# Optimization experiments

Hardware: AMD Instinct MI355X
Metric: run time of the kernel (lower is better)

The kernel has to match this reference:

```python
import jax, jax.numpy as jnp
import numpy as np

B, D, T, K = 32, 256, 1024, 8192


def setup_inputs() -> dict:
    key = jax.random.key(0)
    k1, k2 = jax.random.split(key)
    z_e = jax.random.normal(k1, (B, D, T), dtype=jnp.float32)
    # nn.Embedding init: uniform(-1/K, 1/K)
    emb = jax.random.uniform(k2, (K, D), dtype=jnp.float32, minval=-1.0 / K, maxval=1.0 / K)
    return {"z_e": z_e, "emb": emb}


def reference(z_e, emb):
    b, d, t = z_e.shape
    z_e_f = z_e.astype(jnp.float32)
    # [B, D, T] -> [B*T, D]
    flat = jnp.transpose(z_e_f, (0, 2, 1)).reshape(-1, d)
    # squared L2 distances to every codebook entry: [B*T, K]
    dists = (
        jnp.sum(flat * flat, axis=1, keepdims=True)
        + jnp.sum(emb * emb, axis=1)
        - 2.0 * flat @ emb.T
    )
    idx = jnp.argmin(dists, axis=1)  # [B*T]
    z_q = emb[idx].reshape(b, t, d)  # gather codebook entries
    z_q = jnp.transpose(z_q, (0, 2, 1))  # [B, D, T]
    e_loss = jnp.mean((jax.lax.stop_gradient(z_q) - z_e_f) ** 2)
    # straight-through estimator
    z_q_st = z_e + jax.lax.stop_gradient(z_q - z_e_f)
    return z_q_st, e_loss, idx.reshape(b, t)
```

## Files before the change

### kernel.cpp

```cpp
#include <hip/hip_runtime.h>
#include <stdint.h>

#define BB 32
#define DD 256
#define TT 1024
#define KK 8192

typedef __attribute__((ext_vector_type(2))) float f2;
typedef __attribute__((ext_vector_type(4))) float f4;
typedef __attribute__((ext_vector_type(8))) _Float16 hfrag;
typedef __attribute__((ext_vector_type(16))) float f16acc;

#if __has_builtin(__builtin_elementwise_fma)
#define PKFMA(a, b, c) __builtin_elementwise_fma(a, b, c)
#else
static __device__ __forceinline__ f2 pkfma_(f2 a, f2 b, f2 c) {
    f2 r; r.x = __fmaf_rn(a.x, b.x, c.x); r.y = __fmaf_rn(a.y, b.y, c.y); return r;
}
#define PKFMA(a, b, c) pkfma_(a, b, c)
#endif

#define GLD16(gp, lp)                                                          \
    __builtin_amdgcn_global_load_lds(                                          \
        (const __attribute__((address_space(1))) uint32_t*)(gp),               \
        (__attribute__((address_space(3))) uint32_t*)(lp), 16, 0, 0)

#define MU 3.0e-4f
#define BCAP 4096
#define LIST_CAP 1048576
#define INV512 0.001953125f


#define WS_LOSS   0
#define WS_CNT    8
#define WS_BCNT   16
#define WS_BF     1088
#define WS_AF     33856
#define WS_IDX    164928
#define WS_WIN    296000
#define WS_ZT     558144
#define WS_TMIN   34112576
#define WS_BKT    67667008
#define WS_LIST   71861312
#define WS_ZF     76055616
#define WS_EF     92832832
#define WS_NEED   97027136

__device__ __forceinline__ unsigned short h16(float x) {
    _Float16 t = (_Float16)x;
    return __builtin_bit_cast(unsigned short, t);
}

__device__ __forceinline__ float np_sq_sum256(const float* __restrict__ base, int stride) {
    float res[2];
    #pragma unroll
    for (int blk = 0; blk < 2; ++blk) {
        const int o = blk * 128;
        float r[8];
        #pragma unroll
        for (int j = 0; j < 8; ++j) {
            const float x = base[(o + j) * stride];
            r[j] = __fmul_rn(x, x);
        }
        for (int i = 8; i < 128; i += 8) {
            #pragma unroll
            for (int j = 0; j < 8; ++j) {
                const float x = base[(o + i + j) * stride];
                r[j] = __fadd_rn(r[j], __fmul_rn(x, x));
            }
        }
        res[blk] = __fadd_rn(__fadd_rn(__fadd_rn(r[0], r[1]), __fadd_rn(r[2], r[3])),
                             __fadd_rn(__fadd_rn(r[4], r[5]), __fadd_rn(r[6], r[7])));
    }
    return __fadd_rn(res[0], res[1]);
}

__global__ __launch_bounds__(256) void bsum_kernel(const float* __restrict__ emb,
                                                   float* __restrict__ Bf) {
    const int k = blockIdx.x * 256 + threadIdx.x;
    Bf[k] = np_sq_sum256(emb + (size_t)k * DD, 1);
}

__global__ __launch_bounds__(256) void asum_kernel(const float* __restrict__ z_e,
                                                   float* __restrict__ Af) {
    const int n = blockIdx.x * 256 + threadIdx.x;
    const int b = n >> 10, t = n & 1023;
    Af[n] = np_sq_sum256(z_e + ((size_t)b << 18) + t, TT);
}

__global__ __launch_bounds__(256) void fusedz_kernel(const float* __restrict__ z_e,
                                                     float* __restrict__ zt,
                                                     unsigned short* __restrict__ zf,
                                                     float* __restrict__ Af) {
    __shared__ float tile[64 * 261];
    const int tid = threadIdx.x, l = tid & 63, r = tid >> 6;
    const int n0 = blockIdx.x * 64;
    const int b = n0 >> 10, t0 = n0 & 1023;
    for (int d = r; d < DD; d += 4)
        tile[l * 261 + d] = z_e[(size_t)(b * DD + d) * TT + t0 + l];
    __syncthreads();
    {
        const int q = tid >> 2, c0 = (tid & 3) * 64;
        const float* src = &tile[q * 261 + c0];
        float* dzt = zt + (size_t)(n0 + q) * DD + c0;
        #pragma unroll
        for (int i = 0; i < 16; ++i) {
            f4 v;
            v.x = src[4 * i + 0]; v.y = src[4 * i + 1];
            v.z = src[4 * i + 2]; v.w = src[4 * i + 3];
            *(f4*)(dzt + 4 * i) = v;
        }
    }
    {
        const int g0 = n0 >> 5;
        #pragma unroll
        for (int i = 0; i < 8; ++i) {
            const int slot = tid + 256 * i;
            const int g  = slot >> 10;
            const int ks = (slot >> 6) & 15;
            const int ln = slot & 63;
            const int row = g * 32 + (ln & 31);
            const int col = ks * 16 + (ln >> 5) * 8;
            const float* s = &tile[row * 261 + col];
            ushort4 h0, h1;
            h0.x = h16(s[0]); h0.y = h16(s[1]); h0.z = h16(s[2]); h0.w = h16(s[3]);
            h1.x = h16(s[4]); h1.y = h16(s[5]); h1.z = h16(s[6]); h1.w = h16(s[7]);
            unsigned short* dst = zf + (((size_t)(g0 + g) * 16 + ks) * 64 + ln) * 8;
            *(ushort4*)dst       = h0;
            *(ushort4*)(dst + 4) = h1;
        }
    }
    if (tid < 64) Af[n0 + tid] = np_sq_sum256(&tile[tid * 261], 1);
}

__global__ __launch_bounds__(256) void convef_kernel(const float* __restrict__ emb,
                                                     unsigned short* __restrict__ ef) {
    const int slot = blockIdx.x * 256 + threadIdx.x;
    const int g = slot >> 10, ks = (slot >> 6) & 15, ln = slot & 63;
    const int k = g * 32 + (ln & 31);
    const int d = ks * 16 + (ln >> 5) * 8;
    const float* s = emb + (size_t)k * DD + d;
    const f4 v0 = *(const f4*)s;
    const f4 v1 = *(const f4*)(s + 4);
    ushort4 h0, h1;
    h0.x = h16(v0.x * 1024.0f); h0.y = h16(v0.y * 1024.0f);
    h0.z = h16(v0.z * 1024.0f); h0.w = h16(v0.w * 1024.0f);
    h1.x = h16(v1.x * 1024.0f); h1.y = h16(v1.y * 1024.0f);
    h1.z = h16(v1.z * 1024.0f); h1.w = h16(v1.w * 1024.0f);
    unsigned short* dst = ef + (size_t)slot * 8;
    *(ushort4*)dst       = h0;
    *(ushort4*)(dst + 4) = h1;
}

__device__ __forceinline__ void epi32(const f16acc acc, const float* BfLp,
                                      float (*minbuf)[17], int bfbase, int qrow,
                                      int col, float afv, int lane) {
    const f4 b0 = *(const f4*)&BfLp[bfbase];
    const f4 b1 = *(const f4*)&BfLp[bfbase + 8];
    const f4 b2 = *(const f4*)&BfLp[bfbase + 16];
    const f4 b3 = *(const f4*)&BfLp[bfbase + 24];
    float m =    __fmaf_rn(acc[0],  -INV512, b0.x);
    m = fminf(m, __fmaf_rn(acc[1],  -INV512, b0.y));
    m = fminf(m, __fmaf_rn(acc[2],  -INV512, b0.z));
    m = fminf(m, __fmaf_rn(acc[3],  -INV512, b0.w));
    m = fminf(m, __fmaf_rn(acc[4],  -INV512, b1.x));
    m = fminf(m, __fmaf_rn(acc[5],  -INV512, b1.y));
    m = fminf(m, __fmaf_rn(acc[6],  -INV512, b1.z));
    m = fminf(m, __fmaf_rn(acc[7],  -INV512, b1.w));
    m = fminf(m, __fmaf_rn(acc[8],  -INV512, b2.x));
    m = fminf(m, __fmaf_rn(acc[9],  -INV512, b2.y));
    m = fminf(m, __fmaf_rn(acc[10], -INV512, b2.z));
    m = fminf(m, __fmaf_rn(acc[11], -INV512, b2.w));
    m = fminf(m, __fmaf_rn(acc[12], -INV512, b3.x));
    m = fminf(m, __fmaf_rn(acc[13], -INV512, b3.y));
    m = fminf(m, __fmaf_rn(acc[14], -INV512, b3.z));
    m = fminf(m, __fmaf_rn(acc[15], -INV512, b3.w));
    m = fminf(m, __shfl_xor(m, 32));
    if (lane < 32) minbuf[qrow][col] = afv + m;
}

__global__ __launch_bounds__(256, 2) void mfma1_kernel(
    const unsigned short* __restrict__ zf, const unsigned short* __restrict__ ef,
    const float* __restrict__ Af, const float* __restrict__ Bf,
    float* __restrict__ tmp_min) {
    __shared__ unsigned short Bb[32768];
    __shared__ float minbuf[128][17];
    __shared__ float BfL[512];

    const int tid  = threadIdx.x;
    const int lane = tid & 63;
    const int w    = tid >> 6;
    const int l31  = lane & 31;
    const int hf   = lane >> 5;
    const int wq   = w & 1;
    const int wk   = w >> 1;
    const int qt   = blockIdx.x >> 4;
    const int kb   = blockIdx.x & 15;

    BfL[tid]       = Bf[kb * 512 + tid];
    BfL[tid + 256] = Bf[kb * 512 + 256 + tid];

    hfrag zr[2][16];
    #pragma unroll
    for (int cg = 0; cg < 2; ++cg) {
        const unsigned short* zb =
            zf + (((size_t)(qt * 4 + wq * 2 + cg) * 16) * 64 + lane) * 8;
        #pragma unroll
        for (int ks = 0; ks < 16; ++ks)
            zr[cg][ks] = *(const hfrag*)(zb + (size_t)ks * 512);
    }
    const float af0 = Af[qt * 128 + wq * 64 + l31];
    const float af1 = Af[qt * 128 + wq * 64 + 32 + l31];

    const unsigned short* esrc =
        ef + (((size_t)(kb * 16 + w) * 16) * 64 + lane) * 8;
    #pragma unroll
    for (int ks = 0; ks < 16; ++ks)
        GLD16(esrc + ks * 512, Bb + (w * 16 + ks) * 512);
    __syncthreads();

    for (int kt = 0; kt < 4; ++kt) {
        f16acc acc00 = {}, acc01 = {}, acc10 = {}, acc11 = {};
        #pragma unroll
        for (int ks = 0; ks < 16; ++ks) {
            const hfrag e0 = *(const hfrag*)(Bb + ((wk * 2 + 0) * 16 + ks) * 512 + lane * 8);
            const hfrag e1 = *(const hfrag*)(Bb + ((wk * 2 + 1) * 16 + ks) * 512 + lane * 8);
            acc00 = __builtin_amdgcn_mfma_f32_32x32x16_f16(e0, zr[0][ks], acc00, 0, 0, 0);
            acc01 = __builtin_amdgcn_mfma_f32_32x32x16_f16(e0, zr[1][ks], acc01, 0, 0, 0);
            acc10 = __builtin_amdgcn_mfma_f32_32x32x16_f16(e1, zr[0][ks], acc10, 0, 0, 0);
            acc11 = __builtin_amdgcn_mfma_f32_32x32x16_f16(e1, zr[1][ks], acc11, 0, 0, 0);
        }
        __syncthreads();
        if (kt < 3) {
            const unsigned short* esn = esrc + (size_t)(kt + 1) * 4 * 16 * 512;
            #pragma unroll
            for (int ks = 0; ks < 16; ++ks)
                GLD16(esn + ks * 512, Bb + (w * 16 + ks) * 512);
        }
        {
            const int bfb0 = kt * 128 + (wk * 2 + 0) * 32 + hf * 4;
            const int bfb1 = kt * 128 + (wk * 2 + 1) * 32 + hf * 4;
            const int qr0 = wq * 64 + l31, qr1 = wq * 64 + 32 + l31;
            const int c0 = kt * 4 + wk * 2, c1 = c0 + 1;
            epi32(acc00, BfL, minbuf, bfb0, qr0, c0, af0, lane);
            epi32(acc01, BfL, minbuf, bfb0, qr1, c0, af1, lane);
            epi32(acc10, BfL, minbuf, bfb1, qr0, c1, af0, lane);
            epi32(acc11, BfL, minbuf, bfb1, qr1, c1, af1, lane);
        }
        if (kt < 3) __syncthreads();
    }
    __syncthreads();
    {
        const int qloc = tid >> 1, h8 = (tid & 1) * 8;
        const float* mrow = &minbuf[qloc][h8];
        f4 v0, v1;
        v0.x = mrow[0]; v0.y = mrow[1]; v0.z = mrow[2]; v0.w = mrow[3];
        v1.x = mrow[4]; v1.y = mrow[5]; v1.z = mrow[6]; v1.w = mrow[7];
        float* dst = tmp_min + (size_t)(qt * 128 + qloc) * 256 + kb * 16 + h8;
        *(f4*)dst       = v0;
        *(f4*)(dst + 4) = v1;
    }
}

__global__ __launch_bounds__(256) void select_kernel(
    const float* __restrict__ tmp_min, int* __restrict__ bcnt,
    int* __restrict__ bucket, int* __restrict__ list, int* __restrict__ cnt,
    unsigned long long* __restrict__ winner) {
    const int tid = threadIdx.x, lane = tid & 63, w = tid >> 6;
    const int q = blockIdx.x * 4 + w;
    const f4 v = *(const f4*)(tmp_min + (size_t)q * 256 + lane * 4);
    float m = fminf(fminf(v.x, v.y), fminf(v.z, v.w));
    #pragma unroll
    for (int off = 1; off < 64; off <<= 1) m = fminf(m, __shfl_xor(m, off));
    const float thr = m + MU;
    if (lane == 0) winner[q] = ~0ULL;
    float vv[4] = {v.x, v.y, v.z, v.w};
    #pragma unroll
    for (int j = 0; j < 4; ++j) {
        if (vv[j] <= thr) {
            const int g = lane * 4 + j;
            const int pos = atomicAdd(&bcnt[g], 1);
            if (pos < BCAP) bucket[g * BCAP + pos] = q;
            else {
                const int op = atomicAdd(cnt, 1);
                if (op < LIST_CAP) list[op] = (q << 8) | g;
            }
        }
    }
}

__global__ __launch_bounds__(256) void rescan_bucket_kernel(
    const float* __restrict__ zt, const float* __restrict__ emb,
    const float* __restrict__ Af, const float* __restrict__ Bf,
    const int* __restrict__ bcnt, const int* __restrict__ bucket,
    unsigned long long* __restrict__ winner) {
    __shared__ float elds[256 * 33];
    __shared__ float zbuf[8][256];
    __shared__ float bfs[32];
    const int g     = blockIdx.x >> 3;
    const int slice = blockIdx.x & 7;
    const int tid = threadIdx.x, lane = tid & 63, w = tid >> 6;
    const int half = lane >> 5, l32 = lane & 31, slot = w * 2 + half;
    {
        const int k = tid >> 3, s0 = (tid & 7) * 32;
        const float* src = emb + (size_t)(g * 32 + k) * DD + s0;
        #pragma unroll
        for (int i = 0; i < 8; ++i) {
            const f4 v = *(const f4*)(src + i * 4);
            elds[(s0 + 4 * i + 0) * 33 + k] = v.x;
            elds[(s0 + 4 * i + 1) * 33 + k] = v.y;
            elds[(s0 + 4 * i + 2) * 33 + k] = v.z;
            elds[(s0 + 4 * i + 3) * 33 + k] = v.w;
        }
        if (tid < 32) bfs[tid] = Bf[g * 32 + tid];
    }
    __syncthreads();
    const int nit = min(bcnt[g], BCAP);
    const int kme = g * 32 + l32;
    for (int it = slice * 8 + slot; it < nit; it += 64) {
        const int q = bucket[g * BCAP + it];
        {
            f4* zb = (f4*)&zbuf[slot][0];
            const f4* zsrc = (const f4*)(zt + (size_t)q * DD);
            zb[l32]      = zsrc[l32];
            zb[l32 + 32] = zsrc[l32 + 32];
        }
        const float* zp = &zbuf[slot][0];
        float c = 0.0f;
        #pragma unroll 8
        for (int d = 0; d < DD; ++d)
            c = __fmaf_rn(zp[d], elds[d * 33 + l32], c);
        float bv = __fsub_rn(__fadd_rn(Af[q], bfs[l32]), __fadd_rn(c, c));
        int bk = kme;
        #pragma unroll
        for (int off = 1; off < 32; off <<= 1) {
            const float ob = __shfl_xor(bv, off);
            const int   ok = __shfl_xor(bk, off);
            if (ob < bv || (ob == bv && ok < bk)) { bv = ob; bk = ok; }
        }
        if (l32 == 0)
            atomicMin(winner + q,
                      (((unsigned long long)__float_as_uint(bv)) << 32) | (unsigned)bk);
    }
}

__global__ __launch_bounds__(256) void rescan2_kernel(
    const float* __restrict__ zt, const float* __restrict__ emb,
    const float* __restrict__ Af, const float* __restrict__ Bf,
    const int* __restrict__ list, const int* __restrict__ cnt,
    unsigned long long* __restrict__ winner) {
    __shared__ float zbuf[8][256];
    const int tid = threadIdx.x, lane = tid & 63, w = tid >> 6;
    const int half = lane >> 5, l32 = lane & 31;
    const int slot = blockIdx.x * 8 + w * 2 + half;
    const int slots = gridDim.x * 8;
    const int n = min(*cnt, LIST_CAP);
    f4* zb = (f4*)&zbuf[w * 2 + half][0];
    for (int it = slot; it < n; it += slots) {
        const int id = list[it];
        const int q = id >> 8, g = id & 255;
        const f4* zsrc = (const f4*)(zt + (size_t)q * DD);
        zb[l32]      = zsrc[l32];
        zb[l32 + 32] = zsrc[l32 + 32];
        const int k = g * 32 + l32;
        const f4* e = (const f4*)(emb + (size_t)k * DD);
        float c = 0.0f;
        #pragma unroll 8
        for (int i = 0; i < 64; ++i) {
            const f4 ev = e[i];
            const f4 zv = zb[i];
            c = __fmaf_rn(zv.x, ev.x, c);
            c = __fmaf_rn(zv.y, ev.y, c);
            c = __fmaf_rn(zv.z, ev.z, c);
            c = __fmaf_rn(zv.w, ev.w, c);
        }
        float bv = __fsub_rn(__fadd_rn(Af[q], Bf[k]), __fadd_rn(c, c));
        int bk = k;
        #pragma unroll
        for (int off = 1; off < 32; off <<= 1) {
            const float ob = __shfl_xor(bv, off);
            const int   ok = __shfl_xor(bk, off);
            if (ob < bv || (ob == bv && ok < bk)) { bv = ob; bk = ok; }
        }
        if (l32 == 0)
            atomicMin(winner + q,
                      (((unsigned long long)__float_as_uint(bv)) << 32) | (unsigned)bk);
    }
}

__global__ __launch_bounds__(256) void final_kernel(
    const unsigned long long* __restrict__ winner, float* __restrict__ out_idx,
    int* __restrict__ idx_i, double* __restrict__ loss_acc) {
    __shared__ double ls[4];
    const int tid = threadIdx.x, lane = tid & 63, w = tid >> 6;
    const int q = blockIdx.x * 256 + tid;
    const unsigned long long wv = winner[q];
    const int k = (int)(wv & 0xFFFFFFFFu);
    idx_i[q] = k;
    out_idx[q] = (float)k;
    double s = (double)__uint_as_float((unsigned)(wv >> 32));
    #pragma unroll
    for (int off = 1; off < 64; off <<= 1) s += __shfl_xor(s, off);
    if (lane == 0) ls[w] = s;
    __syncthreads();
    if (tid == 0) atomicAdd(loss_acc, ls[0] + ls[1] + ls[2] + ls[3]);
}

__device__ __forceinline__ void ldstage(const float* __restrict__ emb, int st,
                                        int c, int p, f4* g) {
    const int kt = st >> 4, dc = st & 15;
    const float* src = emb + (((size_t)(kt * 512 + p * 128 + c)) << 8) + dc * 16;
    #pragma unroll
    for (int m = 0; m < 4; ++m) g[m] = *(const f4*)(src + 4 * m);
    const float* src2 = src + (64 << 8);
    #pragma unroll
    for (int m = 0; m < 4; ++m) g[4 + m] = *(const f4*)(src2 + 4 * m);
}

__global__ __launch_bounds__(256, 2) void score5_kernel(
    const float* __restrict__ z_e, const float* __restrict__ emb,
    const float* __restrict__ Bf, const float* __restrict__ Af,
    float* __restrict__ out_idx, int* __restrict__ idx_i,
    double* __restrict__ loss_acc) {
    __shared__ float zl[32 * 260];
    __shared__ float etp[64 * 132];
    const int tid = threadIdx.x;
    const int lane = tid & 63;
    const int w = tid >> 6;
    const int n0 = blockIdx.x * 32;
    const int b = n0 >> 10, t0 = n0 & 1023;
    {
        const int q = tid & 31;
        for (int d = tid >> 5; d < DD; d += 8)
            zl[q * 260 + d] = z_e[((size_t)(b * DD + d) << 10) + t0 + q];
    }
    float Aq[8];
    #pragma unroll
    for (int j = 0; j < 8; ++j) Aq[j] = Af[n0 + w * 8 + j];
    float best[8];
    int bidx[8];
    #pragma unroll
    for (int j = 0; j < 8; ++j) { best[j] = 3.0e38f; bidx[j] = 0; }
    f4 g[8];
    ldstage(emb, 0, lane, w, g);
    for (int kt = 0; kt < 16; ++kt) {
        f2 acc[8][4];
        #pragma unroll
        for (int j = 0; j < 8; ++j)
            #pragma unroll
            for (int p2 = 0; p2 < 4; ++p2) acc[j][p2] = (f2){0.0f, 0.0f};
        for (int dc = 0; dc < 16; ++dc) {
            __syncthreads();
            {
                float* dst = etp + lane * 132 + w * 32;
                #pragma unroll
                for (int m = 0; m < 4; ++m) {
                    const f4 a = g[m], bv = g[4 + m];
                    *(f4*)(dst + 8 * m)     = __builtin_shufflevector(a, bv, 0, 4, 1, 5);
                    *(f4*)(dst + 8 * m + 4) = __builtin_shufflevector(a, bv, 2, 6, 3, 7);
                }
            }
            __syncthreads();
            const int st = kt * 16 + dc;
            ldstage(emb, st < 255 ? st + 1 : 255, lane, w, g);
            #pragma unroll
            for (int s4 = 0; s4 < 4; ++s4) {
                const int dd0 = s4 * 4;
                f4 zv[8];
                #pragma unroll
                for (int j = 0; j < 8; ++j)
                    zv[j] = *(const f4*)(zl + (w * 8 + j) * 260 + dc * 16 + dd0);
                f4 ev[4][2];
                #pragma unroll
                for (int p2 = 0; p2 < 4; ++p2) {
                    const float* eb = etp + lane * 132 + p2 * 32 + dd0 * 2;
                    ev[p2][0] = *(const f4*)(eb);
                    ev[p2][1] = *(const f4*)(eb + 4);
                }
                #pragma unroll
                for (int j = 0; j < 8; ++j) {
                    #pragma unroll
                    for (int dd = 0; dd < 4; ++dd) {
                        const float zs = zv[j][dd];
                        const f2 z2 = {zs, zs};
                        #pragma unroll
                        for (int p2 = 0; p2 < 4; ++p2) {
                            const f4 evv = ev[p2][dd >> 1];
                            const f2 e2 = (dd & 1)
                                ? __builtin_shufflevector(evv, evv, 2, 3)
                                : __builtin_shufflevector(evv, evv, 0, 1);
                            acc[j][p2] = PKFMA(z2, e2, acc[j][p2]);
                        }
                    }
                }
            }
        }
        const int kt0 = kt * 512;
        float Bk[8];
        #pragma unroll
        for (int i = 0; i < 8; ++i) Bk[i] = Bf[kt0 + 64 * i + lane];
        #pragma unroll
        for (int p2 = 0; p2 < 4; ++p2) {
            #pragma unroll
            for (int s = 0; s < 2; ++s) {
                const int i = 2 * p2 + s;
                #pragma unroll
                for (int j = 0; j < 8; ++j) {
                    const float C = s ? acc[j][p2].y : acc[j][p2].x;
                    const float dist = __fsub_rn(__fadd_rn(Aq[j], Bk[i]), __fadd_rn(C, C));
                    const int k = kt0 + 64 * i + lane;
                    if (dist < best[j]) { best[j] = dist; bidx[j] = k; }
                }
            }
        }
    }
    #pragma unroll
    for (int j = 0; j < 8; ++j) {
        float bb = best[j];
        int bi = bidx[j];
        #pragma unroll
        for (int off = 1; off < 64; off <<= 1) {
            const float ob = __shfl_xor(bb, off);
            const int oi = __shfl_xor(bi, off);
            if (ob < bb || (ob == bb && oi < bi)) { bb = ob; bi = oi; }
        }
        best[j] = bb; bidx[j] = bi;
    }
    if (lane == 0) {
        double lp = 0.0;
        #pragma unroll
        for (int j = 0; j < 8; ++j) {
            const int n = n0 + w * 8 + j;
            out_idx[n] = (float)bidx[j];
            idx_i[n] = bidx[j];
            lp += (double)best[j];
        }
        atomicAdd(loss_acc, lp);
    }
}

__global__ __launch_bounds__(256) void gather_kernel(const float* __restrict__ emb,
                                                     const int* __restrict__ idx_i,
                                                     float* __restrict__ zq) {
    const int blk = blockIdx.x;
    const int b = blk >> 4;
    const int t0 = (blk & 15) * 64;
    const int q = threadIdx.x & 63;
    const int dc = threadIdx.x >> 6;
    const int n = b * TT + t0 + q;
    const int k = idx_i[n];
    const f4* erow = (const f4*)(emb + (size_t)k * DD + dc * 64);
    #pragma unroll
    for (int jj = 0; jj < 16; ++jj) {
        const f4 v = erow[jj];
        const int d = dc * 64 + jj * 4;
        zq[(size_t)(b * DD + d + 0) * TT + t0 + q] = v.x;
        zq[(size_t)(b * DD + d + 1) * TT + t0 + q] = v.y;
        zq[(size_t)(b * DD + d + 2) * TT + t0 + q] = v.z;
        zq[(size_t)(b * DD + d + 3) * TT + t0 + q] = v.w;
    }
}

__global__ void fin_kernel(const double* __restrict__ loss_acc,
                           float* __restrict__ out_loss) {
    out_loss[0] = (float)(loss_acc[0] * (1.0 / ((double)BB * DD * TT)));
}

extern "C" void kernel_launch(void* const* d_in, const int* in_sizes, int n_in,
                              void* d_out, int out_size, void* d_ws, size_t ws_size,
                              hipStream_t stream) {
    const float* z_e = (const float*)d_in[0];
    const float* emb = (const float*)d_in[1];

    float* out      = (float*)d_out;
    float* zq       = out;
    float* out_loss = out + (size_t)BB * DD * TT;
    float* out_idx  = out_loss + 1;

    char* ws = (char*)d_ws;
    double* loss_acc = (double*)(ws + WS_LOSS);
    float*  Bf       = (float*)(ws + WS_BF);
    float*  Af       = (float*)(ws + WS_AF);
    int*    idx_i    = (int*)(ws + WS_IDX);

    hipMemsetAsync(d_ws, 0, 1088, stream);
    bsum_kernel<<<KK / 256, 256, 0, stream>>>(emb, Bf);

    if (ws_size >= (size_t)WS_NEED) {
        int*    cnt    = (int*)(ws + WS_CNT);
        int*    bcnt   = (int*)(ws + WS_BCNT);
        unsigned long long* winner = (unsigned long long*)(ws + WS_WIN);
        float*  zt     = (float*)(ws + WS_ZT);
        float*  tmp_min = (float*)(ws + WS_TMIN);
        int*    bucket = (int*)(ws + WS_BKT);
        int*    list   = (int*)(ws + WS_LIST);
        unsigned short* zf = (unsigned short*)(ws + WS_ZF);
        unsigned short* ef = (unsigned short*)(ws + WS_EF);

        fusedz_kernel<<<(BB * TT) / 64, 256, 0, stream>>>(z_e, zt, zf, Af);
        convef_kernel<<<(KK * DD / 8) / 256, 256, 0, stream>>>(emb, ef);
        mfma1_kernel<<<(BB * TT / 128) * 16, 256, 0, stream>>>(zf, ef, Af, Bf, tmp_min);
        select_kernel<<<(BB * TT) / 4, 256, 0, stream>>>(tmp_min, bcnt, bucket, list, cnt, winner);
        rescan_bucket_kernel<<<256 * 8, 256, 0, stream>>>(zt, emb, Af, Bf, bcnt, bucket, winner);
        rescan2_kernel<<<128, 256, 0, stream>>>(zt, emb, Af, Bf, list, cnt, winner);
        final_kernel<<<(BB * TT) / 256, 256, 0, stream>>>(winner, out_idx, idx_i, loss_acc);
    } else {
        asum_kernel<<<(BB * TT) / 256, 256, 0, stream>>>(z_e, Af);
        score5_kernel<<<(BB * TT) / 32, 256, 0, stream>>>(z_e, emb, Bf, Af, out_idx, idx_i, loss_acc);
    }

    gather_kernel<<<(BB * TT) / 64, 256, 0, stream>>>(emb, idx_i, zq);
    fin_kernel<<<1, 1, 0, stream>>>(loss_acc, out_loss);
}
```

Baseline: 400.9 us.

## Double-buffer codebook tiles in MFMA kernel and split rescan across more blocks

Restructures the fp16 MFMA distance kernel so codebook tiles stream through a double-buffered LDS ring in eight phases. Each phase issues the next tile's global-to-LDS loads before computing, with explicit vmcnt waits, raw barriers and raised wave priority around the MFMA loop, so load latency overlaps compute instead of stalling between tiles. Each wave now covers one 32-wide codebook group per phase rather than two. The bucket rescan kernel also gets twice as many blocks per codebook group to add parallelism, at the cost of redundant codebook staging into LDS.

```diff
diff --git a/kernel.cpp b/kernel.cpp
--- a/kernel.cpp
+++ b/kernel.cpp
@@ -183,7 +183,7 @@
     const unsigned short* __restrict__ zf, const unsigned short* __restrict__ ef,
     const float* __restrict__ Af, const float* __restrict__ Bf,
     float* __restrict__ tmp_min) {
-    __shared__ unsigned short Bb[32768];
+    __shared__ unsigned short Bb[2 * 16384];
     __shared__ float minbuf[128][17];
     __shared__ float BfL[512];
 
@@ -193,7 +193,7 @@
     const int l31  = lane & 31;
     const int hf   = lane >> 5;
     const int wq   = w & 1;
-    const int wk   = w >> 1;
+    const int wcg  = w >> 1;
     const int qt   = blockIdx.x >> 4;
     const int kb   = blockIdx.x & 15;
 
@@ -212,43 +212,51 @@
     const float af0 = Af[qt * 128 + wq * 64 + l31];
     const float af1 = Af[qt * 128 + wq * 64 + 32 + l31];
 
-    const unsigned short* esrc =
-        ef + (((size_t)(kb * 16 + w) * 16) * 64 + lane) * 8;
-    #pragma unroll
-    for (int ks = 0; ks < 16; ++ks)
-        GLD16(esrc + ks * 512, Bb + (w * 16 + ks) * 512);
     __syncthreads();
-
-    for (int kt = 0; kt < 4; ++kt) {
-        f16acc acc00 = {}, acc01 = {}, acc10 = {}, acc11 = {};
+    __builtin_amdgcn_sched_barrier(0);
+
+    const unsigned short* esw =
+        ef + ((size_t)(kb * 16 + wcg) * 16 + (w & 1) * 8) * 512 + (size_t)lane * 8;
+    unsigned short* dsw = Bb + (wcg * 16 + (w & 1) * 8) * 512;
+
+    #define STAGE(p) do {                                                      \
+        const unsigned short* s_ =                                             \
+            esw + (size_t)(((p) >> 1) * 4 + ((p) & 1) * 2) * 8192;             \
+        unsigned short* d_ = dsw + ((p) & 1) * 16384;                          \
+        _Pragma("unroll")                                                      \
+        for (int i_ = 0; i_ < 8; ++i_)                                         \
+            GLD16(s_ + i_ * 512, d_ + i_ * 512);                               \
+    } while (0)
+
+    STAGE(0);
+
+    #pragma unroll
+    for (int ph = 0; ph < 8; ++ph) {
+        if (ph < 7) STAGE(ph + 1);
+        if (ph < 7) asm volatile("s_waitcnt vmcnt(8)" ::: "memory");
+        else        asm volatile("s_waitcnt vmcnt(0)" ::: "memory");
+        __builtin_amdgcn_s_barrier();
+        __builtin_amdgcn_sched_barrier(0);
+        const unsigned short* bp = Bb + (ph & 1) * 16384 + wcg * 8192;
+        f16acc a0 = {}, a1 = {};
+        __builtin_amdgcn_s_setprio(1);
         #pragma unroll
         for (int ks = 0; ks < 16; ++ks) {
-            const hfrag e0 = *(const hfrag*)(Bb + ((wk * 2 + 0) * 16 + ks) * 512 + lane * 8);
-            const hfrag e1 = *(const hfrag*)(Bb + ((wk * 2 + 1) * 16 + ks) * 512 + lane * 8);
-            acc00 = __builtin_amdgcn_mfma_f32_32x32x16_f16(e0, zr[0][ks], acc00, 0, 0, 0);
-            acc01 = __builtin_amdgcn_mfma_f32_32x32x16_f16(e0, zr[1][ks], acc01, 0, 0, 0);
-            acc10 = __builtin_amdgcn_mfma_f32_32x32x16_f16(e1, zr[0][ks], acc10, 0, 0, 0);
-            acc11 = __builtin_amdgcn_mfma_f32_32x32x16_f16(e1, zr[1][ks], acc11, 0, 0, 0);
-        }
-        __syncthreads();
-        if (kt < 3) {
-            const unsigned short* esn = esrc + (size_t)(kt + 1) * 4 * 16 * 512;
-            #pragma unroll
-            for (int ks = 0; ks < 16; ++ks)
-                GLD16(esn + ks * 512, Bb + (w * 16 + ks) * 512);
-        }
+            const hfrag e = *(const hfrag*)(bp + ks * 512 + (size_t)lane * 8);
+            a0 = __builtin_amdgcn_mfma_f32_32x32x16_f16(e, zr[0][ks], a0, 0, 0, 0);
+            a1 = __builtin_amdgcn_mfma_f32_32x32x16_f16(e, zr[1][ks], a1, 0, 0, 0);
+        }
+        __builtin_amdgcn_s_setprio(0);
+        __builtin_amdgcn_sched_barrier(0);
+        __builtin_amdgcn_s_barrier();
         {
-            const int bfb0 = kt * 128 + (wk * 2 + 0) * 32 + hf * 4;
-            const int bfb1 = kt * 128 + (wk * 2 + 1) * 32 + hf * 4;
-            const int qr0 = wq * 64 + l31, qr1 = wq * 64 + 32 + l31;
-            const int c0 = kt * 4 + wk * 2, c1 = c0 + 1;
-            epi32(acc00, BfL, minbuf, bfb0, qr0, c0, af0, lane);
-            epi32(acc01, BfL, minbuf, bfb0, qr1, c0, af1, lane);
-            epi32(acc10, BfL, minbuf, bfb1, qr0, c1, af0, lane);
-            epi32(acc11, BfL, minbuf, bfb1, qr1, c1, af1, lane);
-        }
-        if (kt < 3) __syncthreads();
-    }
+            const int gl = (ph >> 1) * 4 + (ph & 1) * 2 + wcg;
+            epi32(a0, BfL, minbuf, gl * 32 + hf * 4, wq * 64 + l31,      gl, af0, lane);
+            epi32(a1, BfL, minbuf, gl * 32 + hf * 4, wq * 64 + 32 + l31, gl, af1, lane);
+        }
+    }
+    #undef STAGE
+
     __syncthreads();
     {
         const int qloc = tid >> 1, h8 = (tid & 1) * 8;
@@ -297,8 +305,8 @@
     __shared__ float elds[256 * 33];
     __shared__ float zbuf[8][256];
     __shared__ float bfs[32];
-    const int g     = blockIdx.x >> 3;
-    const int slice = blockIdx.x & 7;
+    const int g     = blockIdx.x >> 4;
+    const int slice = blockIdx.x & 15;
     const int tid = threadIdx.x, lane = tid & 63, w = tid >> 6;
     const int half = lane >> 5, l32 = lane & 31, slot = w * 2 + half;
     {
@@ -317,7 +325,7 @@
     __syncthreads();
     const int nit = min(bcnt[g], BCAP);
     const int kme = g * 32 + l32;
-    for (int it = slice * 8 + slot; it < nit; it += 64) {
+    for (int it = slice * 8 + slot; it < nit; it += 128) {
         const int q = bucket[g * BCAP + it];
         {
             f4* zb = (f4*)&zbuf[slot][0];
@@ -601,7 +609,7 @@
         convef_kernel<<<(KK * DD / 8) / 256, 256, 0, stream>>>(emb, ef);
         mfma1_kernel<<<(BB * TT / 128) * 16, 256, 0, stream>>>(zf, ef, Af, Bf, tmp_min);
         select_kernel<<<(BB * TT) / 4, 256, 0, stream>>>(tmp_min, bcnt, bucket, list, cnt, winner);
-        rescan_bucket_kernel<<<256 * 8, 256, 0, stream>>>(zt, emb, Af, Bf, bcnt, bucket, winner);
+        rescan_bucket_kernel<<<256 * 16, 256, 0, stream>>>(zt, emb, Af, Bf, bcnt, bucket, winner);
         rescan2_kernel<<<128, 256, 0, stream>>>(zt, emb, Af, Bf, list, cnt, winner);
         final_kernel<<<(BB * TT) / 256, 256, 0, stream>>>(winner, out_idx, idx_i, loss_acc);
     } else {
```

New measurement: 411.3 us. 2.6% more time.
